# Kernel optimization log

Measured on AMD Instinct MI355X. Metric: run time of the kernel, lower is better.

The kernel has to match this reference:

```python
import jax, jax.numpy as jnp
import numpy as np


def setup_inputs() -> dict:
    key = jax.random.key(0)
    k1, k2, k3 = jax.random.split(key, 3)
    N, C, Nf, W, H = 8, 256, 16, 28, 28
    l = jax.random.normal(k1, (N, C, Nf, W, H), dtype=jnp.float32)
    g = jax.random.normal(k2, (N, C, 1, 1, 1), dtype=jnp.float32)
    # 1x1x1 Conv3d(in=C, out=1, bias=False) weight collapses to a length-C vector
    w = jax.random.normal(k3, (C,), dtype=jnp.float32) * (1.0 / np.sqrt(C))
    return {"l": l, "g": g, "w": w}


def reference(l, g, w):
    # l: [N,C,Nf,W,H], g broadcastable to l, w: [C]
    N, C, Nf, W, H = l.shape
    # compatibility score: channel dot-product (1x1x1 conv, out_channels=1)
    c = jnp.einsum('ncfwh,c->nfwh', l + g, w)                      # [N,Nf,W,H]
    # softmax over the spatial dims (W*H) per frame, normalize_attn=True
    a = jax.nn.softmax(c.reshape(N, Nf, W * H), axis=-1)           # [N,Nf,WH]
    a = a.reshape(N, Nf, W, H)
    # attention-weighted spatial sum pooling -> [N,C,Nf]
    g_out = jnp.einsum('nfwh,ncfwh->ncf', a, l)
    # module returns raw compatibility map (pre-softmax) squeezed, and pooled g
    return (c, g_out)
```

## Files before the change

kernel.cpp:

```cpp
#include <hip/hip_runtime.h>
#include <math.h>

constexpr int N_ = 8, C_ = 256, F_ = 16, WH_ = 784;
constexpr int CH_STRIDE = F_ * WH_;
constexpr int COUT_SZ = N_ * F_ * WH_;
constexpr int TILE = 56;
constexpr int NT = 7;
constexpr int LSTR = 60;
constexpr int F4PT = TILE / 4;
constexpr int STAGE_TOT = C_ * F4PT;

__device__ inline float wave_reduce_sum(float v) {
#pragma unroll
  for (int o = 32; o > 0; o >>= 1) v += __shfl_down(v, o, 64);
  return v;
}

__global__ __launch_bounds__(1024) void fused_kernel(
    const float* __restrict__ l, const float* __restrict__ g,
    const float* __restrict__ w, float* __restrict__ out,
    float* __restrict__ ws) {
  __shared__ float buf[C_ * LSTR];
  __shared__ float w_s[C_];
  __shared__ float e_s[TILE];
  __shared__ float red_s[16];
  __shared__ float gb_s;

  const int bid = blockIdx.x;
  const int nf = bid >> 1, ph = bid & 1;
  const int n = nf >> 4, f = nf & 15;
  const int tid = threadIdx.x;
  const int lane = tid & 63, wv = tid >> 6;

  if (tid < C_) w_s[tid] = w[tid];
  float gv = (tid < C_) ? g[n * C_ + tid] * w[tid] : 0.f;
  gv = wave_reduce_sum(gv);
  if (lane == 0) red_s[wv] = gv;
  __syncthreads();
  if (tid == 0) {
    float s = 0.f;
#pragma unroll
    for (int i = 0; i < 16; ++i) s += red_s[i];
    gb_s = s;
  }
  __syncthreads();
  const float gb = gb_s;

  int offG[4], offL[4];
  bool act[4];
#pragma unroll
  for (int k = 0; k < 4; ++k) {
    const int idx = k * 1024 + tid;
    act[k] = (k < 3) || (tid < 512);
    const int c = act[k] ? (idx / F4PT) : 0;
    const int j = idx - c * F4PT;
    offG[k] = c * CH_STRIDE + (j << 2);
    offL[k] = c * LSTR + (j << 2);
  }
  const size_t gbase =
      (size_t)n * (C_ * CH_STRIDE) + (size_t)f * WH_ + ph * 392;

  float4 st[4];
#pragma unroll
  for (int k = 0; k < 4; ++k)
    if (act[k]) st[k] = *reinterpret_cast<const float4*>(l + gbase + offG[k]);

  float gacc = 0.f;
  float s_part = 0.f;
  const int gc = tid >> 2, q = tid & 3;
  const int p = tid >> 3, s8 = tid & 7;

  for (int t = 0; t < NT; ++t) {
#pragma unroll
    for (int k = 0; k < 4; ++k)
      if (act[k]) *reinterpret_cast<float4*>(&buf[offL[k]]) = st[k];
    __syncthreads();

    if (t + 1 < NT) {
      const float* lp = l + gbase + (t + 1) * TILE;
#pragma unroll
      for (int k = 0; k < 4; ++k)
        if (act[k]) st[k] = *reinterpret_cast<const float4*>(lp + offG[k]);
    }

    if (tid < TILE * 8) {
      float acc = 0.f;
#pragma unroll
      for (int k = 0; k < 32; ++k) {
        const int c = s8 + (k << 3);
        acc = fmaf(buf[c * LSTR + p], w_s[c], acc);
      }
      acc += __shfl_down(acc, 4, 64);
      acc += __shfl_down(acc, 2, 64);
      acc += __shfl_down(acc, 1, 64);
      if (s8 == 0) {
        const float cp = acc + gb;
        out[nf * WH_ + ph * 392 + t * TILE + p] = cp;
        const float e = __expf(cp);
        e_s[p] = e;
        s_part += e;
      }
    }
    __syncthreads();

    {
      const int pb = q * F4PT;
#pragma unroll
      for (int j = 0; j < 14; ++j)
        gacc = fmaf(buf[gc * LSTR + pb + j], e_s[pb + j], gacc);
    }
    __syncthreads();
  }

  gacc += __shfl_down(gacc, 2, 64);
  gacc += __shfl_down(gacc, 1, 64);
  if (q == 0) ws[bid * C_ + gc] = gacc;

  float sp = wave_reduce_sum(s_part);
  if (lane == 0) red_s[wv] = sp;
  __syncthreads();
  if (tid == 0) {
    float ssum = 0.f;
#pragma unroll
    for (int i = 0; i < 16; ++i) ssum += red_s[i];
    ws[65536 + bid] = ssum;
  }
}

__global__ __launch_bounds__(1024) void combine_kernel(
    float* __restrict__ out, const float* __restrict__ ws) {
  const int tg = blockIdx.x * 1024 + threadIdx.x;
  const int nf = tg >> 8, c = tg & 255;
  const int n = nf >> 4, f = nf & 15;
  const float G = ws[(2 * nf) * C_ + c] + ws[(2 * nf + 1) * C_ + c];
  const float S = ws[65536 + 2 * nf] + ws[65536 + 2 * nf + 1];
  out[COUT_SZ + (size_t)(n * C_ + c) * F_ + f] = G / S;
}

extern "C" void kernel_launch(void* const* d_in, const int* in_sizes, int n_in,
                              void* d_out, int out_size, void* d_ws,
                              size_t ws_size, hipStream_t stream) {
  const float* l = (const float*)d_in[0];
  const float* g = (const float*)d_in[1];
  const float* w = (const float*)d_in[2];
  float* out = (float*)d_out;
  float* ws = (float*)d_ws;
  fused_kernel<<<dim3(2 * N_ * F_), dim3(1024), 0, stream>>>(l, g, w, out, ws);
  combine_kernel<<<dim3(32), dim3(1024), 0, stream>>>(out, ws);
}
```

Baseline: 179.3 us.

## Split each frame's spatial range into four blocks and drop register prefetch

The grid goes from two to four blocks per (n,f) frame, so each block handles 196 spatial positions in 28-wide tiles. Shared memory per block shrinks and a launch-bounds occupancy hint is added. The register-staged prefetch of the next tile is removed, and loads now go straight to LDS each iteration. The aim is to fill more CUs (512 blocks instead of 256) and raise occupancy, at the cost of losing load/compute overlap inside a block and a four-way partial combine.

```diff
diff --git a/kernel.cpp b/kernel.cpp
--- a/kernel.cpp
+++ b/kernel.cpp
@@ -4,11 +4,12 @@
 constexpr int N_ = 8, C_ = 256, F_ = 16, WH_ = 784;
 constexpr int CH_STRIDE = F_ * WH_;
 constexpr int COUT_SZ = N_ * F_ * WH_;
-constexpr int TILE = 56;
+constexpr int QP = 196;
+constexpr int TILE = 28;
 constexpr int NT = 7;
-constexpr int LSTR = 60;
+constexpr int LSTR = 36;
 constexpr int F4PT = TILE / 4;
-constexpr int STAGE_TOT = C_ * F4PT;
+constexpr int SOFF = 512 * C_;
 
 __device__ inline float wave_reduce_sum(float v) {
 #pragma unroll
@@ -16,7 +17,7 @@
   return v;
 }
 
-__global__ __launch_bounds__(1024) void fused_kernel(
+__global__ __launch_bounds__(1024, 8) void fused_kernel(
     const float* __restrict__ l, const float* __restrict__ g,
     const float* __restrict__ w, float* __restrict__ out,
     float* __restrict__ ws) {
@@ -27,7 +28,7 @@
   __shared__ float gb_s;
 
   const int bid = blockIdx.x;
-  const int nf = bid >> 1, ph = bid & 1;
+  const int nf = bid >> 2, qh = bid & 3;
   const int n = nf >> 4, f = nf & 15;
   const int tid = threadIdx.x;
   const int lane = tid & 63, wv = tid >> 6;
@@ -46,67 +47,61 @@
   __syncthreads();
   const float gb = gb_s;
 
-  int offG[4], offL[4];
-  bool act[4];
-#pragma unroll
-  for (int k = 0; k < 4; ++k) {
-    const int idx = k * 1024 + tid;
-    act[k] = (k < 3) || (tid < 512);
-    const int c = act[k] ? (idx / F4PT) : 0;
-    const int j = idx - c * F4PT;
-    offG[k] = c * CH_STRIDE + (j << 2);
-    offL[k] = c * LSTR + (j << 2);
-  }
+  const int idx0 = tid;
+  const int c0s = idx0 / F4PT, j0 = idx0 - c0s * F4PT;
+  const int og0 = c0s * CH_STRIDE + (j0 << 2);
+  const int ol0 = c0s * LSTR + (j0 << 2);
+  const int idx1 = 1024 + tid;
+  const int c1s = idx1 / F4PT, j1 = idx1 - c1s * F4PT;
+  const int og1 = c1s * CH_STRIDE + (j1 << 2);
+  const int ol1 = c1s * LSTR + (j1 << 2);
+  const bool a1 = (tid < 768);
   const size_t gbase =
-      (size_t)n * (C_ * CH_STRIDE) + (size_t)f * WH_ + ph * 392;
+      (size_t)n * (C_ * CH_STRIDE) + (size_t)f * WH_ + qh * QP;
 
-  float4 st[4];
-#pragma unroll
-  for (int k = 0; k < 4; ++k)
-    if (act[k]) st[k] = *reinterpret_cast<const float4*>(l + gbase + offG[k]);
+  const int p16 = tid >> 4, s16 = tid & 15;
+  const int gc = tid >> 2, q = tid & 3;
 
   float gacc = 0.f;
   float s_part = 0.f;
-  const int gc = tid >> 2, q = tid & 3;
-  const int p = tid >> 3, s8 = tid & 7;
 
   for (int t = 0; t < NT; ++t) {
-#pragma unroll
-    for (int k = 0; k < 4; ++k)
-      if (act[k]) *reinterpret_cast<float4*>(&buf[offL[k]]) = st[k];
+    {
+      const float* lp = l + gbase + t * TILE;
+      const float4 v0 = *reinterpret_cast<const float4*>(lp + og0);
+      if (a1) {
+        const float4 v1 = *reinterpret_cast<const float4*>(lp + og1);
+        *reinterpret_cast<float4*>(&buf[ol1]) = v1;
+      }
+      *reinterpret_cast<float4*>(&buf[ol0]) = v0;
+    }
     __syncthreads();
 
-    if (t + 1 < NT) {
-      const float* lp = l + gbase + (t + 1) * TILE;
-#pragma unroll
-      for (int k = 0; k < 4; ++k)
-        if (act[k]) st[k] = *reinterpret_cast<const float4*>(lp + offG[k]);
-    }
-
-    if (tid < TILE * 8) {
+    if (tid < TILE * 16) {
       float acc = 0.f;
 #pragma unroll
-      for (int k = 0; k < 32; ++k) {
-        const int c = s8 + (k << 3);
-        acc = fmaf(buf[c * LSTR + p], w_s[c], acc);
+      for (int k = 0; k < 16; ++k) {
+        const int c = s16 + (k << 4);
+        acc = fmaf(buf[c * LSTR + p16], w_s[c], acc);
       }
+      acc += __shfl_down(acc, 8, 64);
       acc += __shfl_down(acc, 4, 64);
       acc += __shfl_down(acc, 2, 64);
       acc += __shfl_down(acc, 1, 64);
-      if (s8 == 0) {
+      if (s16 == 0) {
         const float cp = acc + gb;
-        out[nf * WH_ + ph * 392 + t * TILE + p] = cp;
+        out[nf * WH_ + qh * QP + t * TILE + p16] = cp;
         const float e = __expf(cp);
-        e_s[p] = e;
+        e_s[p16] = e;
         s_part += e;
       }
     }
     __syncthreads();
 
     {
-      const int pb = q * F4PT;
+      const int pb = q * 7;
 #pragma unroll
-      for (int j = 0; j < 14; ++j)
+      for (int j = 0; j < 7; ++j)
         gacc = fmaf(buf[gc * LSTR + pb + j], e_s[pb + j], gacc);
     }
     __syncthreads();
@@ -123,7 +118,7 @@
     float ssum = 0.f;
 #pragma unroll
     for (int i = 0; i < 16; ++i) ssum += red_s[i];
-    ws[65536 + bid] = ssum;
+    ws[SOFF + bid] = ssum;
   }
 }
 
@@ -132,8 +127,11 @@
   const int tg = blockIdx.x * 1024 + threadIdx.x;
   const int nf = tg >> 8, c = tg & 255;
   const int n = nf >> 4, f = nf & 15;
-  const float G = ws[(2 * nf) * C_ + c] + ws[(2 * nf + 1) * C_ + c];
-  const float S = ws[65536 + 2 * nf] + ws[65536 + 2 * nf + 1];
+  const int b0 = nf << 2;
+  const float G = ws[(b0 + 0) * C_ + c] + ws[(b0 + 1) * C_ + c] +
+                  ws[(b0 + 2) * C_ + c] + ws[(b0 + 3) * C_ + c];
+  const float S = ws[SOFF + b0] + ws[SOFF + b0 + 1] +
+                  ws[SOFF + b0 + 2] + ws[SOFF + b0 + 3];
   out[COUT_SZ + (size_t)(n * C_ + c) * F_ + f] = G / S;
 }
 
@@ -145,6 +143,6 @@
   const float* w = (const float*)d_in[2];
   float* out = (float*)d_out;
   float* ws = (float*)d_ws;
-  fused_kernel<<<dim3(2 * N_ * F_), dim3(1024), 0, stream>>>(l, g, w, out, ws);
+  fused_kernel<<<dim3(4 * N_ * F_), dim3(1024), 0, stream>>>(l, g, w, out, ws);
   combine_kernel<<<dim3(32), dim3(1024), 0, stream>>>(out, ws);
 }
```

New measurement: 160.6 us. -10.4%, faster.

## Keep l tiles in registers per wave instead of staging through shared memory

Applied to the files above, without the earlier changes.

Each wave now owns 16 channels and each lane owns one spatial position. The lane loads its channel values straight into registers, double-buffered across 64-position passes. Channel partial dot products are reduced through a small shared array, and the exp-weighted pooling accumulates in per-lane registers. This drops the large shared-memory tile and one barrier per pass, but the global loads become scalar rather than float4, and the final reduction needs 16 wave reductions per wave.

```diff
diff --git a/kernel.cpp b/kernel.cpp
--- a/kernel.cpp
+++ b/kernel.cpp
@@ -4,11 +4,13 @@
 constexpr int N_ = 8, C_ = 256, F_ = 16, WH_ = 784;
 constexpr int CH_STRIDE = F_ * WH_;
 constexpr int COUT_SZ = N_ * F_ * WH_;
-constexpr int TILE = 56;
-constexpr int NT = 7;
-constexpr int LSTR = 60;
-constexpr int F4PT = TILE / 4;
-constexpr int STAGE_TOT = C_ * F4PT;
+constexpr int QP = 392;
+constexpr int PASS_P = 64;
+constexpr int NPASS = 7;
+constexpr int TAILV = QP - (NPASS - 1) * PASS_P;
+constexpr int CPS = 16;
+constexpr int PSTR = 17;
+constexpr int SOFF = 256 * C_;
 
 __device__ inline float wave_reduce_sum(float v) {
 #pragma unroll
@@ -16,21 +18,28 @@
   return v;
 }
 
-__global__ __launch_bounds__(1024) void fused_kernel(
+__global__ __launch_bounds__(1024, 4) void fused_kernel(
     const float* __restrict__ l, const float* __restrict__ g,
     const float* __restrict__ w, float* __restrict__ out,
     float* __restrict__ ws) {
-  __shared__ float buf[C_ * LSTR];
+  __shared__ float part[2][PASS_P][PSTR];
   __shared__ float w_s[C_];
-  __shared__ float e_s[TILE];
   __shared__ float red_s[16];
   __shared__ float gb_s;
 
   const int bid = blockIdx.x;
-  const int nf = bid >> 1, ph = bid & 1;
+  const int nf = bid >> 1, half = bid & 1;
   const int n = nf >> 4, f = nf & 15;
   const int tid = threadIdx.x;
   const int lane = tid & 63, wv = tid >> 6;
+
+  const size_t gbase =
+      (size_t)n * (C_ * CH_STRIDE) + (size_t)f * WH_ + half * QP;
+  const float* lb = l + gbase + (size_t)(wv * CPS) * CH_STRIDE + lane;
+
+  float lv[2][CPS];
+#pragma unroll
+  for (int k = 0; k < CPS; ++k) lv[0][k] = lb[(size_t)k * CH_STRIDE];
 
   if (tid < C_) w_s[tid] = w[tid];
   float gv = (tid < C_) ? g[n * C_ + tid] * w[tid] : 0.f;
@@ -46,84 +55,65 @@
   __syncthreads();
   const float gb = gb_s;
 
-  int offG[4], offL[4];
-  bool act[4];
+  float wc[CPS];
 #pragma unroll
-  for (int k = 0; k < 4; ++k) {
-    const int idx = k * 1024 + tid;
-    act[k] = (k < 3) || (tid < 512);
-    const int c = act[k] ? (idx / F4PT) : 0;
-    const int j = idx - c * F4PT;
-    offG[k] = c * CH_STRIDE + (j << 2);
-    offL[k] = c * LSTR + (j << 2);
-  }
-  const size_t gbase =
-      (size_t)n * (C_ * CH_STRIDE) + (size_t)f * WH_ + ph * 392;
+  for (int k = 0; k < CPS; ++k) wc[k] = w_s[wv * CPS + k];
 
-  float4 st[4];
+  float gacc[CPS];
 #pragma unroll
-  for (int k = 0; k < 4; ++k)
-    if (act[k]) st[k] = *reinterpret_cast<const float4*>(l + gbase + offG[k]);
+  for (int k = 0; k < CPS; ++k) gacc[k] = 0.f;
+  float s_part = 0.f;
 
-  float gacc = 0.f;
-  float s_part = 0.f;
-  const int gc = tid >> 2, q = tid & 3;
-  const int p = tid >> 3, s8 = tid & 7;
+#pragma unroll
+  for (int t = 0; t < NPASS; ++t) {
+    const int cb = t & 1, nb = cb ^ 1;
 
-  for (int t = 0; t < NT; ++t) {
+    if (t + 1 < NPASS) {
+      const float* lp = lb + (t + 1) * PASS_P;
+      if (t + 1 == NPASS - 1) {
+        if (lane < TAILV) {
 #pragma unroll
-    for (int k = 0; k < 4; ++k)
-      if (act[k]) *reinterpret_cast<float4*>(&buf[offL[k]]) = st[k];
+          for (int k = 0; k < CPS; ++k) lv[nb][k] = lp[(size_t)k * CH_STRIDE];
+        } else {
+#pragma unroll
+          for (int k = 0; k < CPS; ++k) lv[nb][k] = 0.f;
+        }
+      } else {
+#pragma unroll
+        for (int k = 0; k < CPS; ++k) lv[nb][k] = lp[(size_t)k * CH_STRIDE];
+      }
+    }
+
+    float pc = 0.f;
+#pragma unroll
+    for (int k = 0; k < CPS; ++k) pc = fmaf(lv[cb][k], wc[k], pc);
+    part[cb][lane][wv] = pc;
     __syncthreads();
 
-    if (t + 1 < NT) {
-      const float* lp = l + gbase + (t + 1) * TILE;
+    float rs = 0.f;
 #pragma unroll
-      for (int k = 0; k < 4; ++k)
-        if (act[k]) st[k] = *reinterpret_cast<const float4*>(lp + offG[k]);
+    for (int j = 0; j < 16; ++j) rs += part[cb][lane][j];
+    const bool act = (t < NPASS - 1) || (lane < TAILV);
+    const float cp = rs + gb;
+    float e = 0.f;
+    if (act) {
+      e = __expf(cp);
+      if (wv == 0) out[nf * WH_ + half * QP + t * PASS_P + lane] = cp;
     }
+    if (wv == 0) s_part += e;
 
-    if (tid < TILE * 8) {
-      float acc = 0.f;
 #pragma unroll
-      for (int k = 0; k < 32; ++k) {
-        const int c = s8 + (k << 3);
-        acc = fmaf(buf[c * LSTR + p], w_s[c], acc);
-      }
-      acc += __shfl_down(acc, 4, 64);
-      acc += __shfl_down(acc, 2, 64);
-      acc += __shfl_down(acc, 1, 64);
-      if (s8 == 0) {
-        const float cp = acc + gb;
-        out[nf * WH_ + ph * 392 + t * TILE + p] = cp;
-        const float e = __expf(cp);
-        e_s[p] = e;
-        s_part += e;
-      }
-    }
-    __syncthreads();
-
-    {
-      const int pb = q * F4PT;
-#pragma unroll
-      for (int j = 0; j < 14; ++j)
-        gacc = fmaf(buf[gc * LSTR + pb + j], e_s[pb + j], gacc);
-    }
-    __syncthreads();
+    for (int k = 0; k < CPS; ++k) gacc[k] = fmaf(e, lv[cb][k], gacc[k]);
   }
 
-  gacc += __shfl_down(gacc, 2, 64);
-  gacc += __shfl_down(gacc, 1, 64);
-  if (q == 0) ws[bid * C_ + gc] = gacc;
-
-  float sp = wave_reduce_sum(s_part);
-  if (lane == 0) red_s[wv] = sp;
-  __syncthreads();
-  if (tid == 0) {
-    float ssum = 0.f;
 #pragma unroll
-    for (int i = 0; i < 16; ++i) ssum += red_s[i];
-    ws[65536 + bid] = ssum;
+  for (int k = 0; k < CPS; ++k) {
+    const float r = wave_reduce_sum(gacc[k]);
+    if (lane == 0) ws[bid * C_ + wv * CPS + k] = r;
+  }
+  if (wv == 0) {
+    const float sp = wave_reduce_sum(s_part);
+    if (lane == 0) ws[SOFF + bid] = sp;
   }
 }
 
@@ -132,8 +122,9 @@
   const int tg = blockIdx.x * 1024 + threadIdx.x;
   const int nf = tg >> 8, c = tg & 255;
   const int n = nf >> 4, f = nf & 15;
-  const float G = ws[(2 * nf) * C_ + c] + ws[(2 * nf + 1) * C_ + c];
-  const float S = ws[65536 + 2 * nf] + ws[65536 + 2 * nf + 1];
+  const int b0 = nf << 1;
+  const float G = ws[(b0 + 0) * C_ + c] + ws[(b0 + 1) * C_ + c];
+  const float S = ws[SOFF + b0] + ws[SOFF + b0 + 1];
   out[COUT_SZ + (size_t)(n * C_ + c) * F_ + f] = G / S;
 }
 
```

Result: faster. 170.6 us (-4.9%).
